# Kernel tuning notes

Measured on AMD Instinct MI355X. Metric: run time of the kernel, lower is better.

The kernel has to match this reference:

```python
import jax, jax.numpy as jnp
import numpy as np


def setup_inputs() -> dict:
    key = jax.random.key(0)
    k1, k2 = jax.random.split(key)
    N, D = 8192, 200
    preds = jax.random.normal(k1, (N, 1, 1, D), dtype=jnp.float32)
    labels = jax.random.randint(k2, (N,), 0, 64, dtype=jnp.int64)
    return {"preds": preds, "labels": labels}


def reference(preds, labels):
    # preds: (N,1,1,200) -> flatten to (N,200); torch.dist is the L2 norm of the
    # elementwise difference over the whole tensor.
    N = preds.shape[0]
    x = preds.reshape(N, -1).astype(jnp.float32)
    sq = jnp.sum(x * x, axis=-1)                      # (N,)
    gram = x @ x.T                                    # (N,N)
    d2 = sq[:, None] + sq[None, :] - 2.0 * gram       # squared pairwise dist
    eye = jnp.eye(N, dtype=bool)
    # keep diagonal out of the sqrt (it is skipped by the i==j continue)
    d2_safe = jnp.where(eye, 1.0, jnp.maximum(d2, 0.0))
    dist = jnp.sqrt(d2_safe)                          # (N,N)
    sign = jnp.where(labels[:, None] == labels[None, :], 1.0, -1.0)
    sign = jnp.where(eye, 0.0, sign)
    # each pred_loss[i] is a (1,1,200) tensor filled with the scalar s_i,
    # so the final mean over the stack equals mean_i(s_i).
    per_i = jnp.sum(sign * dist, axis=1)              # (N,)
    return jnp.mean(per_i)
```

## Files before the change

### kernel.cpp

```cpp
#include <hip/hip_runtime.h>
#include <hip/hip_bf16.h>
#include <hip/hip_fp8.h>

#define N 8192
#define D 200
#define KP 232
#define NSTEP 7
#define NB 64
#define NTRI (NB * (NB + 1) / 2)
#define NPART (NTRI * 4)
#define PANEL (128 * KP)

typedef float f32x4 __attribute__((ext_vector_type(4)));
#define AS3 __attribute__((address_space(3)))
#define AS1 __attribute__((address_space(1)))

__global__ __launch_bounds__(256) void prep_kernel(
    const float* __restrict__ x, const int* __restrict__ labels,
    unsigned char* __restrict__ xb, float* __restrict__ sq,
    int* __restrict__ lab) {
  int row = blockIdx.x * 4 + (threadIdx.x >> 6);
  int lane = threadIdx.x & 63;
  const float* xr = x + (size_t)row * D;
  unsigned char* xbr = xb + (size_t)row * KP;
  int k0 = lane * 4;
  float4 f = {0.f, 0.f, 0.f, 0.f};
  if (k0 < D) f = *(const float4*)(xr + k0);
  float s = 0.f;
  unsigned char q[4];
  float ff[4] = {f.x, f.y, f.z, f.w};
#pragma unroll
  for (int c = 0; c < 4; ++c) {
    float v = (k0 + c < D) ? ff[c] : 0.f;
    __hip_fp8_e4m3 h(v);
    q[c] = h.__x;
    float fb = (float)h;
    s += fb * fb;
  }
  if (k0 < KP) *(uchar4*)(xbr + k0) = *(uchar4*)q;
#pragma unroll
  for (int m = 32; m; m >>= 1) s += __shfl_xor(s, m);
  if (lane == 0) {
    sq[row] = s;
    lab[row] = labels[row];
  }
}

__global__ __launch_bounds__(256) void gram_kernel(
    const unsigned char* __restrict__ xb, const float* __restrict__ sq,
    const int* __restrict__ lab, double* __restrict__ partial) {
  __shared__ __align__(16) unsigned char sA[PANEL];
  __shared__ __align__(16) unsigned char sB[PANEL];

  const int p = blockIdx.x;
  int bi = (int)((129.0f - __builtin_sqrtf(129.0f * 129.0f - 8.0f * (float)p)) * 0.5f);
  while ((bi + 1) * NB - ((bi + 1) * bi) / 2 <= p) ++bi;
  while (bi * NB - (bi * (bi - 1)) / 2 > p) --bi;
  const int bj = bi + (p - (bi * NB - (bi * (bi - 1)) / 2));
  const bool diag = (bi == bj);

  const int t = threadIdx.x;
  const unsigned char* gA = xb + (size_t)bi * PANEL;
  const unsigned char* gB = xb + (size_t)bj * PANEL;

#pragma unroll
  for (int c = 0; c < 7; ++c) {
    int off = c * 4096 + t * 16;
    __builtin_amdgcn_global_load_lds((const AS1 void*)(gA + off),
                                     (AS3 void*)(sA + off), 16, 0, 0);
  }
  if (t < 64) {
    int off = 28672 + t * 16;
    __builtin_amdgcn_global_load_lds((const AS1 void*)(gA + off),
                                     (AS3 void*)(sA + off), 16, 0, 0);
  }
  if (!diag) {
#pragma unroll
    for (int c = 0; c < 7; ++c) {
      int off = c * 4096 + t * 16;
      __builtin_amdgcn_global_load_lds((const AS1 void*)(gB + off),
                                       (AS3 void*)(sB + off), 16, 0, 0);
    }
    if (t < 64) {
      int off = 28672 + t * 16;
      __builtin_amdgcn_global_load_lds((const AS1 void*)(gB + off),
                                       (AS3 void*)(sB + off), 16, 0, 0);
    }
  }
  __syncthreads();
  const unsigned char* Bs = diag ? sA : sB;

  const int wid = t >> 6, lane = t & 63;
  const int col = lane & 15, quad = lane >> 4;
  const int waveM = (wid >> 1) * 64, waveN = (wid & 1) * 64;
  const int i0 = bi * 128 + waveM;
  const int j0 = bj * 128 + waveN;

  f32x4 acc[4][4] = {};
#pragma unroll
  for (int step = 0; step < NSTEP; ++step) {
    long a[4], b[4];
#pragma unroll
    for (int mi = 0; mi < 4; ++mi)
      a[mi] = *(const long*)(sA + (waveM + mi * 16 + col) * KP + step * 32 + quad * 8);
#pragma unroll
    for (int ni = 0; ni < 4; ++ni)
      b[ni] = *(const long*)(Bs + (waveN + ni * 16 + col) * KP + step * 32 + quad * 8);
#pragma unroll
    for (int mi = 0; mi < 4; ++mi)
#pragma unroll
      for (int ni = 0; ni < 4; ++ni)
        acc[mi][ni] = __builtin_amdgcn_mfma_f32_16x16x32_fp8_fp8(
            a[mi], b[ni], acc[mi][ni], 0, 0, 0);
  }

  int labj[4];
  float sqj[4];
#pragma unroll
  for (int ni = 0; ni < 4; ++ni) {
    int j = j0 + ni * 16 + col;
    labj[ni] = lab[j];
    sqj[ni] = sq[j];
  }
  float rs = 0.f;
  if (!diag) {
#pragma unroll
    for (int mi = 0; mi < 4; ++mi) {
#pragma unroll
      for (int r = 0; r < 4; ++r) {
        int i = i0 + mi * 16 + quad * 4 + r;
        float sqi = sq[i];
        int li = lab[i];
#pragma unroll
        for (int ni = 0; ni < 4; ++ni) {
          float g = acc[mi][ni][r];
          float d2 = fmaxf(fmaf(-2.f, g, sqi + sqj[ni]), 0.f);
          float dist = __builtin_amdgcn_sqrtf(d2);
          rs += (li == labj[ni]) ? dist : -dist;
        }
      }
    }
  } else {
#pragma unroll
    for (int mi = 0; mi < 4; ++mi) {
#pragma unroll
      for (int r = 0; r < 4; ++r) {
        int i = i0 + mi * 16 + quad * 4 + r;
        float sqi = sq[i];
        int li = lab[i];
#pragma unroll
        for (int ni = 0; ni < 4; ++ni) {
          int j = j0 + ni * 16 + col;
          float g = acc[mi][ni][r];
          float d2 = fmaxf(fmaf(-2.f, g, sqi + sqj[ni]), 0.f);
          float dist = __builtin_amdgcn_sqrtf(d2);
          float c = (li == labj[ni]) ? dist : -dist;
          rs += (i == j) ? 0.f : c;
        }
      }
    }
  }
#pragma unroll
  for (int m = 32; m; m >>= 1) rs += __shfl_xor(rs, m);
  if (lane == 0) {
    double w = diag ? 1.0 : 2.0;
    partial[p * 4 + wid] = w * (double)rs;
  }
}

__global__ __launch_bounds__(256) void reduce_kernel(
    const double* __restrict__ partial, float* __restrict__ out) {
  __shared__ double wsum[4];
  double s = 0.0;
  for (int i = threadIdx.x; i < NPART; i += 256) s += partial[i];
#pragma unroll
  for (int m = 32; m; m >>= 1) s += __shfl_xor(s, m);
  if ((threadIdx.x & 63) == 0) wsum[threadIdx.x >> 6] = s;
  __syncthreads();
  if (threadIdx.x == 0)
    out[0] = (float)((wsum[0] + wsum[1] + wsum[2] + wsum[3]) / (double)N);
}

extern "C" void kernel_launch(void* const* d_in, const int* in_sizes, int n_in,
                              void* d_out, int out_size, void* d_ws, size_t ws_size,
                              hipStream_t stream) {
  const float* x = (const float*)d_in[0];
  const int* labels = (const int*)d_in[1];
  char* ws = (char*)d_ws;
  unsigned char* xb = (unsigned char*)ws;
  float* sq = (float*)(ws + (size_t)N * KP);
  int* lab = (int*)(ws + (size_t)N * KP + (size_t)N * 4);
  double* partial = (double*)(ws + (size_t)N * KP + (size_t)N * 8);
  float* out = (float*)d_out;

  prep_kernel<<<N / 4, 256, 0, stream>>>(x, labels, xb, sq, lab);
  gram_kernel<<<NTRI, 256, 0, stream>>>(xb, sq, lab, partial);
  reduce_kernel<<<1, 256, 0, stream>>>(partial, out);
}
```

Baseline: 89.00 us.

## Make gram kernel persistent over paired triangle rows with prefetch overlap

Replaces the one-block-per-tile launch over the upper-triangular tile grid with 512 persistent blocks. Each block walks a balanced pair of triangle rows (q and 63-q), 65 tiles in all, with a stride of 16. While the epilogue of the current tile runs, the next tile's panels are prefetched into LDS, and the A panel is reused when the row index does not change. The intent is to cut per-block launch and load overhead and to hide global-to-LDS latency. In exchange, per-block accumulation now happens in float over many tiles instead of double per tile, and extra barriers are added.

```diff
diff --git a/kernel.cpp b/kernel.cpp
--- a/kernel.cpp
+++ b/kernel.cpp
@@ -7,8 +7,8 @@
 #define KP 232
 #define NSTEP 7
 #define NB 64
-#define NTRI (NB * (NB + 1) / 2)
-#define NPART (NTRI * 4)
+#define NBLK 512
+#define NPART (NBLK * 4)
 #define PANEL (128 * KP)
 
 typedef float f32x4 __attribute__((ext_vector_type(4)));
@@ -52,120 +52,126 @@
   __shared__ __align__(16) unsigned char sA[PANEL];
   __shared__ __align__(16) unsigned char sB[PANEL];
 
-  const int p = blockIdx.x;
-  int bi = (int)((129.0f - __builtin_sqrtf(129.0f * 129.0f - 8.0f * (float)p)) * 0.5f);
-  while ((bi + 1) * NB - ((bi + 1) * bi) / 2 <= p) ++bi;
-  while (bi * NB - (bi * (bi - 1)) / 2 > p) --bi;
-  const int bj = bi + (p - (bi * NB - (bi * (bi - 1)) / 2));
-  const bool diag = (bi == bj);
-
   const int t = threadIdx.x;
-  const unsigned char* gA = xb + (size_t)bi * PANEL;
-  const unsigned char* gB = xb + (size_t)bj * PANEL;
-
-#pragma unroll
-  for (int c = 0; c < 7; ++c) {
-    int off = c * 4096 + t * 16;
-    __builtin_amdgcn_global_load_lds((const AS1 void*)(gA + off),
-                                     (AS3 void*)(sA + off), 16, 0, 0);
-  }
-  if (t < 64) {
-    int off = 28672 + t * 16;
-    __builtin_amdgcn_global_load_lds((const AS1 void*)(gA + off),
-                                     (AS3 void*)(sA + off), 16, 0, 0);
-  }
-  if (!diag) {
-#pragma unroll
-    for (int c = 0; c < 7; ++c) {
-      int off = c * 4096 + t * 16;
-      __builtin_amdgcn_global_load_lds((const AS1 void*)(gB + off),
-                                       (AS3 void*)(sB + off), 16, 0, 0);
-    }
-    if (t < 64) {
-      int off = 28672 + t * 16;
-      __builtin_amdgcn_global_load_lds((const AS1 void*)(gB + off),
-                                       (AS3 void*)(sB + off), 16, 0, 0);
-    }
-  }
-  __syncthreads();
-  const unsigned char* Bs = diag ? sA : sB;
+  const int b = blockIdx.x;
+  const int q = b >> 4, s = b & 15;
+  const int row2 = 63 - q;
+  const int n1 = 64 - q;
 
   const int wid = t >> 6, lane = t & 63;
   const int col = lane & 15, quad = lane >> 4;
   const int waveM = (wid >> 1) * 64, waveN = (wid & 1) * 64;
-  const int i0 = bi * 128 + waveM;
-  const int j0 = bj * 128 + waveN;
-
-  f32x4 acc[4][4] = {};
-#pragma unroll
-  for (int step = 0; step < NSTEP; ++step) {
-    long a[4], b[4];
-#pragma unroll
-    for (int mi = 0; mi < 4; ++mi)
-      a[mi] = *(const long*)(sA + (waveM + mi * 16 + col) * KP + step * 32 + quad * 8);
-#pragma unroll
-    for (int ni = 0; ni < 4; ++ni)
-      b[ni] = *(const long*)(Bs + (waveN + ni * 16 + col) * KP + step * 32 + quad * 8);
-#pragma unroll
-    for (int mi = 0; mi < 4; ++mi)
+
+  auto stage = [&](const unsigned char* g, unsigned char* sh) {
+#pragma unroll
+    for (int c = 0; c < 7; ++c) {
+      int off = c * 4096 + t * 16;
+      __builtin_amdgcn_global_load_lds((const AS1 void*)(g + off),
+                                       (AS3 void*)(sh + off), 16, 0, 0);
+    }
+    if (t < 64) {
+      int off = 28672 + t * 16;
+      __builtin_amdgcn_global_load_lds((const AS1 void*)(g + off),
+                                       (AS3 void*)(sh + off), 16, 0, 0);
+    }
+  };
+
+  int idx = s;
+  int bi = (idx < n1) ? q : row2;
+  int bj = (idx < n1) ? q + idx : row2 + (idx - n1);
+  stage(xb + (size_t)bi * PANEL, sA);
+  stage(xb + (size_t)bj * PANEL, sB);
+  __syncthreads();
+
+  float tot = 0.f;
+  while (true) {
+    f32x4 acc[4][4] = {};
+#pragma unroll
+    for (int step = 0; step < NSTEP; ++step) {
+      long a[4], bf[4];
+#pragma unroll
+      for (int mi = 0; mi < 4; ++mi)
+        a[mi] = *(const long*)(sA + (waveM + mi * 16 + col) * KP + step * 32 + quad * 8);
 #pragma unroll
       for (int ni = 0; ni < 4; ++ni)
-        acc[mi][ni] = __builtin_amdgcn_mfma_f32_16x16x32_fp8_fp8(
-            a[mi], b[ni], acc[mi][ni], 0, 0, 0);
-  }
-
-  int labj[4];
-  float sqj[4];
-#pragma unroll
-  for (int ni = 0; ni < 4; ++ni) {
-    int j = j0 + ni * 16 + col;
-    labj[ni] = lab[j];
-    sqj[ni] = sq[j];
-  }
-  float rs = 0.f;
-  if (!diag) {
-#pragma unroll
-    for (int mi = 0; mi < 4; ++mi) {
-#pragma unroll
-      for (int r = 0; r < 4; ++r) {
-        int i = i0 + mi * 16 + quad * 4 + r;
-        float sqi = sq[i];
-        int li = lab[i];
-#pragma unroll
-        for (int ni = 0; ni < 4; ++ni) {
-          float g = acc[mi][ni][r];
-          float d2 = fmaxf(fmaf(-2.f, g, sqi + sqj[ni]), 0.f);
-          float dist = __builtin_amdgcn_sqrtf(d2);
-          rs += (li == labj[ni]) ? dist : -dist;
+        bf[ni] = *(const long*)(sB + (waveN + ni * 16 + col) * KP + step * 32 + quad * 8);
+#pragma unroll
+      for (int mi = 0; mi < 4; ++mi)
+#pragma unroll
+        for (int ni = 0; ni < 4; ++ni)
+          acc[mi][ni] = __builtin_amdgcn_mfma_f32_16x16x32_fp8_fp8(
+              a[mi], bf[ni], acc[mi][ni], 0, 0, 0);
+    }
+    __syncthreads();
+
+    const int nidx = idx + 16;
+    const bool more = (nidx < 65);
+    int nbi = 0, nbj = 0;
+    if (more) {
+      nbi = (nidx < n1) ? q : row2;
+      nbj = (nidx < n1) ? q + nidx : row2 + (nidx - n1);
+      if (nbi != bi) stage(xb + (size_t)nbi * PANEL, sA);
+      stage(xb + (size_t)nbj * PANEL, sB);
+    }
+
+    const int i0 = bi * 128 + waveM, j0 = bj * 128 + waveN;
+    int labj[4];
+    float sqj[4];
+#pragma unroll
+    for (int ni = 0; ni < 4; ++ni) {
+      int j = j0 + ni * 16 + col;
+      labj[ni] = lab[j];
+      sqj[ni] = sq[j];
+    }
+    float rs = 0.f;
+    if (bi != bj) {
+#pragma unroll
+      for (int mi = 0; mi < 4; ++mi) {
+#pragma unroll
+        for (int r = 0; r < 4; ++r) {
+          int i = i0 + mi * 16 + quad * 4 + r;
+          float sqi = sq[i];
+          int li = lab[i];
+#pragma unroll
+          for (int ni = 0; ni < 4; ++ni) {
+            float g = acc[mi][ni][r];
+            float d2 = fmaxf(fmaf(-2.f, g, sqi + sqj[ni]), 0.f);
+            float dist = __builtin_amdgcn_sqrtf(d2);
+            rs += (li == labj[ni]) ? dist : -dist;
+          }
         }
       }
-    }
-  } else {
-#pragma unroll
-    for (int mi = 0; mi < 4; ++mi) {
-#pragma unroll
-      for (int r = 0; r < 4; ++r) {
-        int i = i0 + mi * 16 + quad * 4 + r;
-        float sqi = sq[i];
-        int li = lab[i];
-#pragma unroll
-        for (int ni = 0; ni < 4; ++ni) {
-          int j = j0 + ni * 16 + col;
-          float g = acc[mi][ni][r];
-          float d2 = fmaxf(fmaf(-2.f, g, sqi + sqj[ni]), 0.f);
-          float dist = __builtin_amdgcn_sqrtf(d2);
-          float c = (li == labj[ni]) ? dist : -dist;
-          rs += (i == j) ? 0.f : c;
+      tot += 2.f * rs;
+    } else {
+#pragma unroll
+      for (int mi = 0; mi < 4; ++mi) {
+#pragma unroll
+        for (int r = 0; r < 4; ++r) {
+          int i = i0 + mi * 16 + quad * 4 + r;
+          float sqi = sq[i];
+          int li = lab[i];
+#pragma unroll
+          for (int ni = 0; ni < 4; ++ni) {
+            int j = j0 + ni * 16 + col;
+            float g = acc[mi][ni][r];
+            float d2 = fmaxf(fmaf(-2.f, g, sqi + sqj[ni]), 0.f);
+            float dist = __builtin_amdgcn_sqrtf(d2);
+            float c = (li == labj[ni]) ? dist : -dist;
+            rs += (i == j) ? 0.f : c;
+          }
         }
       }
-    }
+      tot += rs;
+    }
+
+    if (!more) break;
+    bi = nbi; bj = nbj; idx = nidx;
+    __syncthreads();
   }
-#pragma unroll
-  for (int m = 32; m; m >>= 1) rs += __shfl_xor(rs, m);
-  if (lane == 0) {
-    double w = diag ? 1.0 : 2.0;
-    partial[p * 4 + wid] = w * (double)rs;
-  }
+
+#pragma unroll
+  for (int m = 32; m; m >>= 1) tot += __shfl_xor(tot, m);
+  if (lane == 0) partial[b * 4 + wid] = (double)tot;
 }
 
 __global__ __launch_bounds__(256) void reduce_kernel(
@@ -194,6 +200,6 @@
   float* out = (float*)d_out;
 
   prep_kernel<<<N / 4, 256, 0, stream>>>(x, labels, xb, sq, lab);
-  gram_kernel<<<NTRI, 256, 0, stream>>>(xb, sq, lab, partial);
+  gram_kernel<<<NBLK, 256, 0, stream>>>(xb, sq, lab, partial);
   reduce_kernel<<<1, 256, 0, stream>>>(partial, out);
 }
```

Result: faster. 83.01 us (median of 2 runs) (-6.7%).
